# Performance work log

Hardware: AMD Instinct MI355X
Metric: run time of the kernel (lower is better)

The kernel has to match this reference:

```python
import jax, jax.numpy as jnp
import numpy as np

N_NODES = 100000
N_EDGES = 3200000
HID = 64


def setup_inputs() -> dict:
    key = jax.random.key(0)
    ks = jax.random.split(key, 20)
    x = jax.random.normal(ks[0], (N_NODES, 3), dtype=jnp.float32)
    edge_index = jax.random.randint(ks[1], (2, N_EDGES), 0, N_NODES, dtype=jnp.int32)

    def glorot(k, fan_in, fan_out):
        s = jnp.sqrt(6.0 / (fan_in + fan_out))
        return jax.random.uniform(k, (fan_in, fan_out), jnp.float32, -s, s)

    W_in = glorot(ks[2], 3, HID)
    b_in = jnp.zeros((HID,), jnp.float32)
    W_hid = jnp.stack([glorot(ks[3 + i], HID, HID) for i in range(6)])  # [6,64,64]
    b_hid = jnp.zeros((6, HID), jnp.float32)
    W_out = glorot(ks[10], HID, 6)
    b_out = jnp.zeros((6,), jnp.float32)
    return {"x": x, "edge_index": edge_index, "W_in": W_in, "b_in": b_in,
            "W_hid": W_hid, "b_hid": b_hid, "W_out": W_out, "b_out": b_out}


def _gcn_layer(x, W, b, src, dst, norm):
    # PyG GCNConv: h = x @ W; out[dst] += norm * h[src]; out += b
    h = x @ W
    msg = h[src] * norm[:, None]            # [E+N, F]
    agg = jax.ops.segment_sum(msg, dst, num_segments=N_NODES)
    return agg + b


def reference(x, edge_index, W_in, b_in, W_hid, b_hid, W_out, b_out):
    # Add self-loops and symmetric normalization (computed once, shared by all layers)
    loops = jnp.arange(N_NODES, dtype=edge_index.dtype)
    src = jnp.concatenate([edge_index[0], loops])
    dst = jnp.concatenate([edge_index[1], loops])
    deg = jax.ops.segment_sum(jnp.ones_like(dst, dtype=x.dtype), dst, num_segments=N_NODES)
    dinv = jnp.where(deg > 0, jax.lax.rsqrt(deg), 0.0)
    norm = dinv[src] * dinv[dst]            # [E+N]

    h = jax.nn.relu(_gcn_layer(x, W_in, b_in, src, dst, norm))
    for i in range(6):
        h = jax.nn.relu(_gcn_layer(h, W_hid[i], b_hid[i], src, dst, norm))
    # dropout p=0.25 with train=False -> identity (eval mode)
    out = _gcn_layer(h, W_out, b_out, src, dst, norm)
    return jax.nn.sigmoid(out)
```

## Files before the change

kernel.cpp:

```cpp
#include <hip/hip_runtime.h>
#include <hip/hip_fp16.h>
#include <math.h>

#define MAXBKT 512


__global__ __launch_bounds__(256) void k_bcount(const int* __restrict__ dstA,
                                                int E, int N, int nbkt, int* bucketCnt) {
    __shared__ int cnt[MAXBKT];
    for (int i = threadIdx.x; i < nbkt; i += 256) cnt[i] = 0;
    __syncthreads();
    int total = E + N;
    for (int i = blockIdx.x * 256 + threadIdx.x; i < total; i += gridDim.x * 256) {
        int d = (i < E) ? dstA[i] : (i - E);
        atomicAdd(&cnt[d >> 8], 1);
    }
    __syncthreads();
    for (int i = threadIdx.x; i < nbkt; i += 256)
        if (cnt[i]) atomicAdd(&bucketCnt[i], cnt[i]);
}

__global__ __launch_bounds__(MAXBKT) void k_bscan(const int* __restrict__ bucketCnt,
                                                  int* bucketOff, int* bucketCur,
                                                  int nbkt, int total) {
    __shared__ int sm[MAXBKT];
    int tid = threadIdx.x;
    int v = (tid < nbkt) ? bucketCnt[tid] : 0;
    sm[tid] = v;
    __syncthreads();
    for (int off = 1; off < MAXBKT; off <<= 1) {
        int t = 0;
        if (tid >= off) t = sm[tid - off];
        __syncthreads();
        sm[tid] += t;
        __syncthreads();
    }
    if (tid < nbkt) {
        int excl = sm[tid] - v;
        bucketOff[tid] = excl;
        bucketCur[tid] = excl;
    }
    if (tid == 0) bucketOff[nbkt] = total;
}

__global__ __launch_bounds__(256) void k_bscat2(const int* __restrict__ srcA,
                                                const int* __restrict__ dstA,
                                                int* bucketCur, unsigned int* bedges,
                                                int E, int N, int nbkt, int chunk) {
    __shared__ int cnt[MAXBKT];
    __shared__ int base[MAXBKT];
    int total = E + N;
    int lo = blockIdx.x * chunk;
    int hi = lo + chunk; if (hi > total) hi = total;
    for (int i = threadIdx.x; i < nbkt; i += 256) cnt[i] = 0;
    __syncthreads();
    for (int i = lo + threadIdx.x; i < hi; i += 256) {
        int d = (i < E) ? dstA[i] : (i - E);
        atomicAdd(&cnt[d >> 8], 1);
    }
    __syncthreads();
    for (int i = threadIdx.x; i < nbkt; i += 256) {
        base[i] = cnt[i] ? atomicAdd(&bucketCur[i], cnt[i]) : 0;
        cnt[i] = 0;
    }
    __syncthreads();
    for (int i = lo + threadIdx.x; i < hi; i += 256) {
        int s, d;
        if (i < E) { s = srcA[i]; d = dstA[i]; }
        else       { s = d = i - E; }
        int b = d >> 8;
        int pos = base[b] + atomicAdd(&cnt[b], 1);
        bedges[pos] = ((unsigned int)(d & 255) << 24) | (unsigned int)s;
    }
}

__global__ __launch_bounds__(256) void k_bfill2(const unsigned int* __restrict__ bedges,
                                                const int* __restrict__ bucketOff,
                                                const float* __restrict__ x,
                                                int* __restrict__ rowptr,
                                                float* __restrict__ dinv,
                                                float* __restrict__ xs,
                                                int* __restrict__ col,
                                                int N, int total) {
    __shared__ int ldeg[256];
    __shared__ int lcur[256];
    int b = blockIdx.x;
    int tid = threadIdx.x;
    int bo = bucketOff[b], be = bucketOff[b + 1];
    ldeg[tid] = 0;
    __syncthreads();
    for (int j = bo + tid; j < be; j += 256)
        atomicAdd(&ldeg[bedges[j] >> 24], 1);
    __syncthreads();
    int dg = ldeg[tid];
    lcur[tid] = dg;
    __syncthreads();
    for (int off = 1; off < 256; off <<= 1) {
        int t = 0;
        if (tid >= off) t = lcur[tid - off];
        __syncthreads();
        lcur[tid] += t;
        __syncthreads();
    }
    int excl = lcur[tid] - dg;
    int node = (b << 8) + tid;
    if (node < N) {
        rowptr[node] = bo + excl;
        float dv = dg > 0 ? rsqrtf((float)dg) : 0.0f;
        dinv[node] = dv;
        xs[node * 3 + 0] = dv * x[node * 3 + 0];
        xs[node * 3 + 1] = dv * x[node * 3 + 1];
        xs[node * 3 + 2] = dv * x[node * 3 + 2];
    }
    if (b == 0 && tid == 0) rowptr[N] = total;
    __syncthreads();
    lcur[tid] = bo + excl;
    __syncthreads();
    for (int j = bo + tid; j < be; j += 256) {
        unsigned int e = bedges[j];
        int pos = atomicAdd(&lcur[e >> 24], 1);
        col[pos] = (int)(e & 0x00FFFFFFu);
    }
}


__global__ __launch_bounds__(256) void k_agg3(const float* __restrict__ xs,
                                              const int* __restrict__ rowptr,
                                              const int* __restrict__ col,
                                              const float* __restrict__ dinv,
                                              float* __restrict__ out3, int n) {
    int i = blockIdx.x * 256 + threadIdx.x;
    if (i >= n) return;
    float a0 = 0.f, a1 = 0.f, a2 = 0.f;
    int beg = rowptr[i], end = rowptr[i + 1];
    for (int j = beg; j < end; ++j) {
        int s = col[j];
        a0 += xs[s * 3 + 0];
        a1 += xs[s * 3 + 1];
        a2 += xs[s * 3 + 2];
    }
    float dv = dinv[i];
    out3[i * 3 + 0] = dv * a0;
    out3[i * 3 + 1] = dv * a1;
    out3[i * 3 + 2] = dv * a2;
}

__global__ __launch_bounds__(512) void k_tin_mm(const float* __restrict__ agg3v,
                                                const float* __restrict__ Win,
                                                const float* __restrict__ bin,
                                                const float* __restrict__ W0,
                                                const float* __restrict__ dinv,
                                                __half* __restrict__ tout, int n) {
    __shared__ float Wl[64 * 64];
    __shared__ float Hl[8][68];
    int tid = threadIdx.x;
    {
        int i = tid * 4;
        *(float4*)&Wl[i] = *(const float4*)&W0[i];
        *(float4*)&Wl[i + 2048] = *(const float4*)&W0[i + 2048];
    }
    int nodeBase = blockIdx.x * 8;
    int nl = tid >> 6, f = tid & 63;
    int node = nodeBase + nl;
    if (node < n) {
        float a0 = agg3v[node * 3 + 0];
        float a1 = agg3v[node * 3 + 1];
        float a2 = agg3v[node * 3 + 2];
        float v = bin[f] + a0 * Win[f] + a1 * Win[64 + f] + a2 * Win[128 + f];
        Hl[nl][f] = fmaxf(v, 0.f);
    }
    __syncthreads();
    if (node < n) {
        float acc = 0.f;
#pragma unroll
        for (int k = 0; k < 64; ++k) acc += Hl[nl][k] * Wl[k * 64 + f];
        tout[(size_t)node * 64 + f] = __float2half(acc * dinv[node]);
    }
}

__global__ __launch_bounds__(512) void k_aggmm64(const __half* __restrict__ tin,
                                                 const int* __restrict__ rowptr,
                                                 const int* __restrict__ col,
                                                 const float* __restrict__ dinv,
                                                 const float* __restrict__ bias,
                                                 const float* __restrict__ W,
                                                 __half* __restrict__ tnext, int n) {
    __shared__ float Wl[64 * 64];
    __shared__ float Hl[8][68];
    int tid = threadIdx.x;
    {
        int i = tid * 4;
        *(float4*)&Wl[i] = *(const float4*)&W[i];
        *(float4*)&Wl[i + 2048] = *(const float4*)&W[i + 2048];
    }
    int nodeBase = blockIdx.x * 8;
    int wv = tid >> 6;
    int lane = tid & 63;
    int slot = lane >> 3;
    int fl = lane & 7;
    int node = nodeBase + wv;
    float a0 = 0.f, a1 = 0.f, a2 = 0.f, a3 = 0.f, a4 = 0.f, a5 = 0.f, a6 = 0.f, a7 = 0.f;
    if (node < n) {
        int beg = rowptr[node], end = rowptr[node + 1];
        int j = beg + slot;
        for (; j + 24 < end; j += 32) {
            int s0 = col[j], s1 = col[j + 8], s2 = col[j + 16], s3 = col[j + 24];
            float4 r0 = *(const float4*)(tin + (size_t)s0 * 64 + fl * 8);
            float4 r1 = *(const float4*)(tin + (size_t)s1 * 64 + fl * 8);
            float4 r2 = *(const float4*)(tin + (size_t)s2 * 64 + fl * 8);
            float4 r3 = *(const float4*)(tin + (size_t)s3 * 64 + fl * 8);
            const __half2* h0 = (const __half2*)&r0;
            const __half2* h1 = (const __half2*)&r1;
            const __half2* h2 = (const __half2*)&r2;
            const __half2* h3 = (const __half2*)&r3;
            float2 p;
            p = __half22float2(h0[0]); a0 += p.x; a1 += p.y;
            p = __half22float2(h0[1]); a2 += p.x; a3 += p.y;
            p = __half22float2(h0[2]); a4 += p.x; a5 += p.y;
            p = __half22float2(h0[3]); a6 += p.x; a7 += p.y;
            p = __half22float2(h1[0]); a0 += p.x; a1 += p.y;
            p = __half22float2(h1[1]); a2 += p.x; a3 += p.y;
            p = __half22float2(h1[2]); a4 += p.x; a5 += p.y;
            p = __half22float2(h1[3]); a6 += p.x; a7 += p.y;
            p = __half22float2(h2[0]); a0 += p.x; a1 += p.y;
            p = __half22float2(h2[1]); a2 += p.x; a3 += p.y;
            p = __half22float2(h2[2]); a4 += p.x; a5 += p.y;
            p = __half22float2(h2[3]); a6 += p.x; a7 += p.y;
            p = __half22float2(h3[0]); a0 += p.x; a1 += p.y;
            p = __half22float2(h3[1]); a2 += p.x; a3 += p.y;
            p = __half22float2(h3[2]); a4 += p.x; a5 += p.y;
            p = __half22float2(h3[3]); a6 += p.x; a7 += p.y;
        }
        for (; j < end; j += 8) {
            int s0 = col[j];
            float4 r0 = *(const float4*)(tin + (size_t)s0 * 64 + fl * 8);
            const __half2* h0 = (const __half2*)&r0;
            float2 p;
            p = __half22float2(h0[0]); a0 += p.x; a1 += p.y;
            p = __half22float2(h0[1]); a2 += p.x; a3 += p.y;
            p = __half22float2(h0[2]); a4 += p.x; a5 += p.y;
            p = __half22float2(h0[3]); a6 += p.x; a7 += p.y;
        }
    }
#pragma unroll
    for (int m = 8; m < 64; m <<= 1) {
        a0 += __shfl_xor(a0, m, 64);
        a1 += __shfl_xor(a1, m, 64);
        a2 += __shfl_xor(a2, m, 64);
        a3 += __shfl_xor(a3, m, 64);
        a4 += __shfl_xor(a4, m, 64);
        a5 += __shfl_xor(a5, m, 64);
        a6 += __shfl_xor(a6, m, 64);
        a7 += __shfl_xor(a7, m, 64);
    }
    if (slot == 0 && node < n) {
        float dv = dinv[node];
        int fo = fl * 8;
        float4 w0, w1;
        w0.x = fmaxf(dv * a0 + bias[fo + 0], 0.f);
        w0.y = fmaxf(dv * a1 + bias[fo + 1], 0.f);
        w0.z = fmaxf(dv * a2 + bias[fo + 2], 0.f);
        w0.w = fmaxf(dv * a3 + bias[fo + 3], 0.f);
        w1.x = fmaxf(dv * a4 + bias[fo + 4], 0.f);
        w1.y = fmaxf(dv * a5 + bias[fo + 5], 0.f);
        w1.z = fmaxf(dv * a6 + bias[fo + 6], 0.f);
        w1.w = fmaxf(dv * a7 + bias[fo + 7], 0.f);
        *(float4*)&Hl[wv][fo] = w0;
        *(float4*)&Hl[wv][fo + 4] = w1;
    }
    __syncthreads();
    if (node < n) {
        int f = lane;
        float acc = 0.f;
#pragma unroll
        for (int k = 0; k < 64; ++k) acc += Hl[wv][k] * Wl[k * 64 + f];
        tnext[(size_t)node * 64 + f] = __float2half(acc * dinv[node]);
    }
}

__global__ __launch_bounds__(512) void k_aggtout(const __half* __restrict__ tin,
                                                 const int* __restrict__ rowptr,
                                                 const int* __restrict__ col,
                                                 const float* __restrict__ dinv,
                                                 const float* __restrict__ bias,
                                                 const float* __restrict__ Wout,
                                                 __half* __restrict__ t6p, int n) {
    __shared__ float Wl6[64 * 6];
    __shared__ float Hl[8][68];
    int tid = threadIdx.x;
    if (tid < 384) Wl6[tid] = Wout[tid];
    int nodeBase = blockIdx.x * 8;
    int wv = tid >> 6;
    int lane = tid & 63;
    int slot = lane >> 3;
    int fl = lane & 7;
    int node = nodeBase + wv;
    float a0 = 0.f, a1 = 0.f, a2 = 0.f, a3 = 0.f, a4 = 0.f, a5 = 0.f, a6 = 0.f, a7 = 0.f;
    if (node < n) {
        int beg = rowptr[node], end = rowptr[node + 1];
        int j = beg + slot;
        for (; j + 24 < end; j += 32) {
            int s0 = col[j], s1 = col[j + 8], s2 = col[j + 16], s3 = col[j + 24];
            float4 r0 = *(const float4*)(tin + (size_t)s0 * 64 + fl * 8);
            float4 r1 = *(const float4*)(tin + (size_t)s1 * 64 + fl * 8);
            float4 r2 = *(const float4*)(tin + (size_t)s2 * 64 + fl * 8);
            float4 r3 = *(const float4*)(tin + (size_t)s3 * 64 + fl * 8);
            const __half2* h0 = (const __half2*)&r0;
            const __half2* h1 = (const __half2*)&r1;
            const __half2* h2 = (const __half2*)&r2;
            const __half2* h3 = (const __half2*)&r3;
            float2 p;
            p = __half22float2(h0[0]); a0 += p.x; a1 += p.y;
            p = __half22float2(h0[1]); a2 += p.x; a3 += p.y;
            p = __half22float2(h0[2]); a4 += p.x; a5 += p.y;
            p = __half22float2(h0[3]); a6 += p.x; a7 += p.y;
            p = __half22float2(h1[0]); a0 += p.x; a1 += p.y;
            p = __half22float2(h1[1]); a2 += p.x; a3 += p.y;
            p = __half22float2(h1[2]); a4 += p.x; a5 += p.y;
            p = __half22float2(h1[3]); a6 += p.x; a7 += p.y;
            p = __half22float2(h2[0]); a0 += p.x; a1 += p.y;
            p = __half22float2(h2[1]); a2 += p.x; a3 += p.y;
            p = __half22float2(h2[2]); a4 += p.x; a5 += p.y;
            p = __half22float2(h2[3]); a6 += p.x; a7 += p.y;
            p = __half22float2(h3[0]); a0 += p.x; a1 += p.y;
            p = __half22float2(h3[1]); a2 += p.x; a3 += p.y;
            p = __half22float2(h3[2]); a4 += p.x; a5 += p.y;
            p = __half22float2(h3[3]); a6 += p.x; a7 += p.y;
        }
        for (; j < end; j += 8) {
            int s0 = col[j];
            float4 r0 = *(const float4*)(tin + (size_t)s0 * 64 + fl * 8);
            const __half2* h0 = (const __half2*)&r0;
            float2 p;
            p = __half22float2(h0[0]); a0 += p.x; a1 += p.y;
            p = __half22float2(h0[1]); a2 += p.x; a3 += p.y;
            p = __half22float2(h0[2]); a4 += p.x; a5 += p.y;
            p = __half22float2(h0[3]); a6 += p.x; a7 += p.y;
        }
    }
#pragma unroll
    for (int m = 8; m < 64; m <<= 1) {
        a0 += __shfl_xor(a0, m, 64);
        a1 += __shfl_xor(a1, m, 64);
        a2 += __shfl_xor(a2, m, 64);
        a3 += __shfl_xor(a3, m, 64);
        a4 += __shfl_xor(a4, m, 64);
        a5 += __shfl_xor(a5, m, 64);
        a6 += __shfl_xor(a6, m, 64);
        a7 += __shfl_xor(a7, m, 64);
    }
    if (slot == 0 && node < n) {
        float dv = dinv[node];
        int fo = fl * 8;
        float4 w0, w1;
        w0.x = fmaxf(dv * a0 + bias[fo + 0], 0.f);
        w0.y = fmaxf(dv * a1 + bias[fo + 1], 0.f);
        w0.z = fmaxf(dv * a2 + bias[fo + 2], 0.f);
        w0.w = fmaxf(dv * a3 + bias[fo + 3], 0.f);
        w1.x = fmaxf(dv * a4 + bias[fo + 4], 0.f);
        w1.y = fmaxf(dv * a5 + bias[fo + 5], 0.f);
        w1.z = fmaxf(dv * a6 + bias[fo + 6], 0.f);
        w1.w = fmaxf(dv * a7 + bias[fo + 7], 0.f);
        *(float4*)&Hl[wv][fo] = w0;
        *(float4*)&Hl[wv][fo + 4] = w1;
    }
    __syncthreads();
    if (node < n && lane < 8) {
        __half o = __float2half(0.f);
        if (lane < 6) {
            float acc = 0.f;
#pragma unroll
            for (int k = 0; k < 64; ++k) acc += Hl[wv][k] * Wl6[k * 6 + lane];
            o = __float2half(acc * dinv[node]);
        }
        t6p[(size_t)node * 8 + lane] = o;
    }
}

__global__ __launch_bounds__(256) void k_agg6(const __half* __restrict__ t6p,
                                              const int* __restrict__ rowptr,
                                              const int* __restrict__ col,
                                              const float* __restrict__ dinv,
                                              const float* __restrict__ bout,
                                              float* __restrict__ out, int n) {
    int i = blockIdx.x * 256 + threadIdx.x;
    if (i >= n) return;
    float a0 = 0.f, a1 = 0.f, a2 = 0.f, a3 = 0.f, a4 = 0.f, a5 = 0.f;
    int beg = rowptr[i], end = rowptr[i + 1];
    int j = beg;
    for (; j + 1 < end; j += 2) {
        int s0 = col[j], s1 = col[j + 1];
        float4 r0 = *(const float4*)(t6p + (size_t)s0 * 8);
        float4 r1 = *(const float4*)(t6p + (size_t)s1 * 8);
        const __half2* h0 = (const __half2*)&r0;
        const __half2* h1 = (const __half2*)&r1;
        float2 p;
        p = __half22float2(h0[0]); a0 += p.x; a1 += p.y;
        p = __half22float2(h0[1]); a2 += p.x; a3 += p.y;
        p = __half22float2(h0[2]); a4 += p.x; a5 += p.y;
        p = __half22float2(h1[0]); a0 += p.x; a1 += p.y;
        p = __half22float2(h1[1]); a2 += p.x; a3 += p.y;
        p = __half22float2(h1[2]); a4 += p.x; a5 += p.y;
    }
    if (j < end) {
        int s0 = col[j];
        float4 r0 = *(const float4*)(t6p + (size_t)s0 * 8);
        const __half2* h0 = (const __half2*)&r0;
        float2 p;
        p = __half22float2(h0[0]); a0 += p.x; a1 += p.y;
        p = __half22float2(h0[1]); a2 += p.x; a3 += p.y;
        p = __half22float2(h0[2]); a4 += p.x; a5 += p.y;
    }
    float dv = dinv[i];
    out[i * 6 + 0] = 1.0f / (1.0f + expf(-(dv * a0 + bout[0])));
    out[i * 6 + 1] = 1.0f / (1.0f + expf(-(dv * a1 + bout[1])));
    out[i * 6 + 2] = 1.0f / (1.0f + expf(-(dv * a2 + bout[2])));
    out[i * 6 + 3] = 1.0f / (1.0f + expf(-(dv * a3 + bout[3])));
    out[i * 6 + 4] = 1.0f / (1.0f + expf(-(dv * a4 + bout[4])));
    out[i * 6 + 5] = 1.0f / (1.0f + expf(-(dv * a5 + bout[5])));
}


extern "C" void kernel_launch(void* const* d_in, const int* in_sizes, int n_in,
                              void* d_out, int out_size, void* d_ws, size_t ws_size,
                              hipStream_t stream) {
    const float* x    = (const float*)d_in[0];
    const int*   eidx = (const int*)d_in[1];
    const float* Win  = (const float*)d_in[2];
    const float* bin  = (const float*)d_in[3];
    const float* Whid = (const float*)d_in[4];
    const float* bhid = (const float*)d_in[5];
    const float* Wout = (const float*)d_in[6];
    const float* bout = (const float*)d_in[7];
    float* out = (float*)d_out;

    const int N = in_sizes[0] / 3;
    const int E = in_sizes[1] / 2;
    const int* srcA = eidx;
    const int* dstA = eidx + E;
    const int TOT = E + N;
    const int NBKT = (N + 255) >> 8;

    char* p = (char*)d_ws;
    auto alloc = [&](size_t bytes) -> void* {
        void* r = (void*)p;
        p += (bytes + 255) & ~(size_t)255;
        return r;
    };
    float*        dinv      = (float*)alloc((size_t)N * 4);
    int*          rowptr    = (int*)alloc((size_t)(N + 1) * 4);
    int*          bucketCnt = (int*)alloc((size_t)MAXBKT * 4);
    int*          bucketOff = (int*)alloc((size_t)(MAXBKT + 1) * 4);
    int*          bucketCur = (int*)alloc((size_t)MAXBKT * 4);
    unsigned int* bedges    = (unsigned int*)alloc((size_t)TOT * 4);
    int*          col       = (int*)alloc((size_t)TOT * 4);
    float*        xs        = (float*)alloc((size_t)N * 3 * 4);
    float*        agg3buf   = (float*)alloc((size_t)N * 3 * 4);
    __half*       tA        = (__half*)alloc((size_t)N * 64 * 2);
    __half*       tB        = (__half*)alloc((size_t)N * 64 * 2);
    __half*       t6p       = (__half*)alloc((size_t)N * 8 * 2);

    const int NB_N = (N + 255) / 256;
    const int NB8  = (N + 7) / 8;

    hipMemsetAsync(bucketCnt, 0, (size_t)MAXBKT * 4, stream);
    k_bcount<<<512, 256, 0, stream>>>(dstA, E, N, NBKT, bucketCnt);
    k_bscan<<<1, MAXBKT, 0, stream>>>(bucketCnt, bucketOff, bucketCur, NBKT, TOT);
    const int CHUNK = (TOT + 511) / 512;
    k_bscat2<<<512, 256, 0, stream>>>(srcA, dstA, bucketCur, bedges, E, N, NBKT, CHUNK);
    k_bfill2<<<NBKT, 256, 0, stream>>>(bedges, bucketOff, x, rowptr, dinv, xs, col, N, TOT);

    k_agg3<<<NB_N, 256, 0, stream>>>(xs, rowptr, col, dinv, agg3buf, N);
    k_tin_mm<<<NB8, 512, 0, stream>>>(agg3buf, Win, bin, Whid, dinv, tA, N);

    __half* tin = tA;
    __half* tnx = tB;
    for (int i = 1; i <= 5; ++i) {
        k_aggmm64<<<NB8, 512, 0, stream>>>(tin, rowptr, col, dinv,
                                           bhid + (size_t)(i - 1) * 64,
                                           Whid + (size_t)i * 4096, tnx, N);
        __half* tmp = tin; tin = tnx; tnx = tmp;
    }

    k_aggtout<<<NB8, 512, 0, stream>>>(tin, rowptr, col, dinv,
                                       bhid + (size_t)5 * 64, Wout, t6p, N);

    k_agg6<<<NB_N, 256, 0, stream>>>(t6p, rowptr, col, dinv, bout, out, N);
}
```

Measured before the change: 770.5 us.

## Keep layer weights in registers and drop shared-memory matmul in fused agg kernels

The fused aggregate+matmul kernels stop staging the 64x64 weight matrix and the aggregated row in LDS. Each lane now holds an 8x8 slice of W (as half2) plus its bias in registers, and computes the per-node transform with a shuffle reduction. This removes the 16KB LDS fill per block and the block-wide barrier, and blocks shrink to 4 nodes of 256 threads. In exchange it adds register pressure, rounds the weights to fp16, and every block re-reads W from global/cache.

```diff
diff --git a/kernel.cpp b/kernel.cpp
--- a/kernel.cpp
+++ b/kernel.cpp
@@ -178,69 +178,72 @@
     }
 }
 
-__global__ __launch_bounds__(512) void k_aggmm64(const __half* __restrict__ tin,
+__global__ __launch_bounds__(256) void k_aggmm64(const __half* __restrict__ tin,
                                                  const int* __restrict__ rowptr,
                                                  const int* __restrict__ col,
                                                  const float* __restrict__ dinv,
                                                  const float* __restrict__ bias,
                                                  const float* __restrict__ W,
                                                  __half* __restrict__ tnext, int n) {
-    __shared__ float Wl[64 * 64];
-    __shared__ float Hl[8][68];
     int tid = threadIdx.x;
-    {
-        int i = tid * 4;
-        *(float4*)&Wl[i] = *(const float4*)&W[i];
-        *(float4*)&Wl[i + 2048] = *(const float4*)&W[i + 2048];
-    }
-    int nodeBase = blockIdx.x * 8;
-    int wv = tid >> 6;
     int lane = tid & 63;
     int slot = lane >> 3;
-    int fl = lane & 7;
-    int node = nodeBase + wv;
+    int fl   = lane & 7;
+    __half2 w2[8][4];
+    float biasreg[8];
+#pragma unroll
+    for (int q = 0; q < 8; ++q) {
+        const float* wrow = W + (fl * 8 + q) * 64 + slot * 8;
+        float4 wa = *(const float4*)wrow;
+        float4 wb = *(const float4*)(wrow + 4);
+        w2[q][0] = __floats2half2_rn(wa.x, wa.y);
+        w2[q][1] = __floats2half2_rn(wa.z, wa.w);
+        w2[q][2] = __floats2half2_rn(wb.x, wb.y);
+        w2[q][3] = __floats2half2_rn(wb.z, wb.w);
+        biasreg[q] = bias[fl * 8 + q];
+    }
+    int node = blockIdx.x * 4 + (tid >> 6);
+    if (node >= n) return;
+    int beg = rowptr[node], end = rowptr[node + 1];
     float a0 = 0.f, a1 = 0.f, a2 = 0.f, a3 = 0.f, a4 = 0.f, a5 = 0.f, a6 = 0.f, a7 = 0.f;
-    if (node < n) {
-        int beg = rowptr[node], end = rowptr[node + 1];
-        int j = beg + slot;
-        for (; j + 24 < end; j += 32) {
-            int s0 = col[j], s1 = col[j + 8], s2 = col[j + 16], s3 = col[j + 24];
-            float4 r0 = *(const float4*)(tin + (size_t)s0 * 64 + fl * 8);
-            float4 r1 = *(const float4*)(tin + (size_t)s1 * 64 + fl * 8);
-            float4 r2 = *(const float4*)(tin + (size_t)s2 * 64 + fl * 8);
-            float4 r3 = *(const float4*)(tin + (size_t)s3 * 64 + fl * 8);
-            const __half2* h0 = (const __half2*)&r0;
-            const __half2* h1 = (const __half2*)&r1;
-            const __half2* h2 = (const __half2*)&r2;
-            const __half2* h3 = (const __half2*)&r3;
-            float2 p;
-            p = __half22float2(h0[0]); a0 += p.x; a1 += p.y;
-            p = __half22float2(h0[1]); a2 += p.x; a3 += p.y;
-            p = __half22float2(h0[2]); a4 += p.x; a5 += p.y;
-            p = __half22float2(h0[3]); a6 += p.x; a7 += p.y;
-            p = __half22float2(h1[0]); a0 += p.x; a1 += p.y;
-            p = __half22float2(h1[1]); a2 += p.x; a3 += p.y;
-            p = __half22float2(h1[2]); a4 += p.x; a5 += p.y;
-            p = __half22float2(h1[3]); a6 += p.x; a7 += p.y;
-            p = __half22float2(h2[0]); a0 += p.x; a1 += p.y;
-            p = __half22float2(h2[1]); a2 += p.x; a3 += p.y;
-            p = __half22float2(h2[2]); a4 += p.x; a5 += p.y;
-            p = __half22float2(h2[3]); a6 += p.x; a7 += p.y;
-            p = __half22float2(h3[0]); a0 += p.x; a1 += p.y;
-            p = __half22float2(h3[1]); a2 += p.x; a3 += p.y;
-            p = __half22float2(h3[2]); a4 += p.x; a5 += p.y;
-            p = __half22float2(h3[3]); a6 += p.x; a7 += p.y;
-        }
-        for (; j < end; j += 8) {
-            int s0 = col[j];
-            float4 r0 = *(const float4*)(tin + (size_t)s0 * 64 + fl * 8);
-            const __half2* h0 = (const __half2*)&r0;
-            float2 p;
-            p = __half22float2(h0[0]); a0 += p.x; a1 += p.y;
-            p = __half22float2(h0[1]); a2 += p.x; a3 += p.y;
-            p = __half22float2(h0[2]); a4 += p.x; a5 += p.y;
-            p = __half22float2(h0[3]); a6 += p.x; a7 += p.y;
-        }
+    int j = beg + slot;
+    for (; j + 24 < end; j += 32) {
+        int s0 = col[j], s1 = col[j + 8], s2 = col[j + 16], s3 = col[j + 24];
+        float4 r0 = *(const float4*)(tin + (size_t)s0 * 64 + fl * 8);
+        float4 r1 = *(const float4*)(tin + (size_t)s1 * 64 + fl * 8);
+        float4 r2 = *(const float4*)(tin + (size_t)s2 * 64 + fl * 8);
+        float4 r3 = *(const float4*)(tin + (size_t)s3 * 64 + fl * 8);
+        const __half2* h0 = (const __half2*)&r0;
+        const __half2* h1 = (const __half2*)&r1;
+        const __half2* h2 = (const __half2*)&r2;
+        const __half2* h3 = (const __half2*)&r3;
+        float2 p;
+        p = __half22float2(h0[0]); a0 += p.x; a1 += p.y;
+        p = __half22float2(h0[1]); a2 += p.x; a3 += p.y;
+        p = __half22float2(h0[2]); a4 += p.x; a5 += p.y;
+        p = __half22float2(h0[3]); a6 += p.x; a7 += p.y;
+        p = __half22float2(h1[0]); a0 += p.x; a1 += p.y;
+        p = __half22float2(h1[1]); a2 += p.x; a3 += p.y;
+        p = __half22float2(h1[2]); a4 += p.x; a5 += p.y;
+        p = __half22float2(h1[3]); a6 += p.x; a7 += p.y;
+        p = __half22float2(h2[0]); a0 += p.x; a1 += p.y;
+        p = __half22float2(h2[1]); a2 += p.x; a3 += p.y;
+        p = __half22float2(h2[2]); a4 += p.x; a5 += p.y;
+        p = __half22float2(h2[3]); a6 += p.x; a7 += p.y;
+        p = __half22float2(h3[0]); a0 += p.x; a1 += p.y;
+        p = __half22float2(h3[1]); a2 += p.x; a3 += p.y;
+        p = __half22float2(h3[2]); a4 += p.x; a5 += p.y;
+        p = __half22float2(h3[3]); a6 += p.x; a7 += p.y;
+    }
+    for (; j < end; j += 8) {
+        int s0 = col[j];
+        float4 r0 = *(const float4*)(tin + (size_t)s0 * 64 + fl * 8);
+        const __half2* h0 = (const __half2*)&r0;
+        float2 p;
+        p = __half22float2(h0[0]); a0 += p.x; a1 += p.y;
+        p = __half22float2(h0[1]); a2 += p.x; a3 += p.y;
+        p = __half22float2(h0[2]); a4 += p.x; a5 += p.y;
+        p = __half22float2(h0[3]); a6 += p.x; a7 += p.y;
     }
 #pragma unroll
     for (int m = 8; m < 64; m <<= 1) {
@@ -253,90 +256,102 @@
         a6 += __shfl_xor(a6, m, 64);
         a7 += __shfl_xor(a7, m, 64);
     }
-    if (slot == 0 && node < n) {
-        float dv = dinv[node];
-        int fo = fl * 8;
-        float4 w0, w1;
-        w0.x = fmaxf(dv * a0 + bias[fo + 0], 0.f);
-        w0.y = fmaxf(dv * a1 + bias[fo + 1], 0.f);
-        w0.z = fmaxf(dv * a2 + bias[fo + 2], 0.f);
-        w0.w = fmaxf(dv * a3 + bias[fo + 3], 0.f);
-        w1.x = fmaxf(dv * a4 + bias[fo + 4], 0.f);
-        w1.y = fmaxf(dv * a5 + bias[fo + 5], 0.f);
-        w1.z = fmaxf(dv * a6 + bias[fo + 6], 0.f);
-        w1.w = fmaxf(dv * a7 + bias[fo + 7], 0.f);
-        *(float4*)&Hl[wv][fo] = w0;
-        *(float4*)&Hl[wv][fo + 4] = w1;
-    }
-    __syncthreads();
-    if (node < n) {
-        int f = lane;
-        float acc = 0.f;
-#pragma unroll
-        for (int k = 0; k < 64; ++k) acc += Hl[wv][k] * Wl[k * 64 + f];
-        tnext[(size_t)node * 64 + f] = __float2half(acc * dinv[node]);
-    }
-}
-
-__global__ __launch_bounds__(512) void k_aggtout(const __half* __restrict__ tin,
+    float dv = dinv[node];
+    float h[8];
+    h[0] = fmaxf(dv * a0 + biasreg[0], 0.f);
+    h[1] = fmaxf(dv * a1 + biasreg[1], 0.f);
+    h[2] = fmaxf(dv * a2 + biasreg[2], 0.f);
+    h[3] = fmaxf(dv * a3 + biasreg[3], 0.f);
+    h[4] = fmaxf(dv * a4 + biasreg[4], 0.f);
+    h[5] = fmaxf(dv * a5 + biasreg[5], 0.f);
+    h[6] = fmaxf(dv * a6 + biasreg[6], 0.f);
+    h[7] = fmaxf(dv * a7 + biasreg[7], 0.f);
+    float acc[8] = {0.f, 0.f, 0.f, 0.f, 0.f, 0.f, 0.f, 0.f};
+#pragma unroll
+    for (int q = 0; q < 8; ++q) {
+        float hq = h[q];
+#pragma unroll
+        for (int p2 = 0; p2 < 4; ++p2) {
+            float2 wf = __half22float2(w2[q][p2]);
+            acc[2 * p2]     += hq * wf.x;
+            acc[2 * p2 + 1] += hq * wf.y;
+        }
+    }
+#pragma unroll
+    for (int m = 1; m < 8; m <<= 1) {
+#pragma unroll
+        for (int p = 0; p < 8; ++p) acc[p] += __shfl_xor(acc[p], m, 64);
+    }
+    if (fl == 0) {
+        __half2 o[4];
+        o[0] = __floats2half2_rn(acc[0] * dv, acc[1] * dv);
+        o[1] = __floats2half2_rn(acc[2] * dv, acc[3] * dv);
+        o[2] = __floats2half2_rn(acc[4] * dv, acc[5] * dv);
+        o[3] = __floats2half2_rn(acc[6] * dv, acc[7] * dv);
+        *(float4*)&tnext[(size_t)node * 64 + slot * 8] = *(float4*)o;
+    }
+}
+
+__global__ __launch_bounds__(256) void k_aggtout(const __half* __restrict__ tin,
                                                  const int* __restrict__ rowptr,
                                                  const int* __restrict__ col,
                                                  const float* __restrict__ dinv,
                                                  const float* __restrict__ bias,
                                                  const float* __restrict__ Wout,
                                                  __half* __restrict__ t6p, int n) {
-    __shared__ float Wl6[64 * 6];
-    __shared__ float Hl[8][68];
     int tid = threadIdx.x;
-    if (tid < 384) Wl6[tid] = Wout[tid];
-    int nodeBase = blockIdx.x * 8;
-    int wv = tid >> 6;
     int lane = tid & 63;
     int slot = lane >> 3;
-    int fl = lane & 7;
-    int node = nodeBase + wv;
+    int fl   = lane & 7;
+    float woutreg[8];
+    float biasreg[8];
+#pragma unroll
+    for (int q = 0; q < 8; ++q) {
+        woutreg[q] = (slot < 6) ? Wout[(fl * 8 + q) * 6 + slot] : 0.f;
+        biasreg[q] = bias[fl * 8 + q];
+    }
+    int node = blockIdx.x * 4 + (tid >> 6);
+    if (node >= n) return;
+    int beg = rowptr[node], end = rowptr[node + 1];
     float a0 = 0.f, a1 = 0.f, a2 = 0.f, a3 = 0.f, a4 = 0.f, a5 = 0.f, a6 = 0.f, a7 = 0.f;
-    if (node < n) {
-        int beg = rowptr[node], end = rowptr[node + 1];
-        int j = beg + slot;
-        for (; j + 24 < end; j += 32) {
-            int s0 = col[j], s1 = col[j + 8], s2 = col[j + 16], s3 = col[j + 24];
-            float4 r0 = *(const float4*)(tin + (size_t)s0 * 64 + fl * 8);
-            float4 r1 = *(const float4*)(tin + (size_t)s1 * 64 + fl * 8);
-            float4 r2 = *(const float4*)(tin + (size_t)s2 * 64 + fl * 8);
-            float4 r3 = *(const float4*)(tin + (size_t)s3 * 64 + fl * 8);
-            const __half2* h0 = (const __half2*)&r0;
-            const __half2* h1 = (const __half2*)&r1;
-            const __half2* h2 = (const __half2*)&r2;
-            const __half2* h3 = (const __half2*)&r3;
-            float2 p;
-            p = __half22float2(h0[0]); a0 += p.x; a1 += p.y;
-            p = __half22float2(h0[1]); a2 += p.x; a3 += p.y;
-            p = __half22float2(h0[2]); a4 += p.x; a5 += p.y;
-            p = __half22float2(h0[3]); a6 += p.x; a7 += p.y;
-            p = __half22float2(h1[0]); a0 += p.x; a1 += p.y;
-            p = __half22float2(h1[1]); a2 += p.x; a3 += p.y;
-            p = __half22float2(h1[2]); a4 += p.x; a5 += p.y;
-            p = __half22float2(h1[3]); a6 += p.x; a7 += p.y;
-            p = __half22float2(h2[0]); a0 += p.x; a1 += p.y;
-            p = __half22float2(h2[1]); a2 += p.x; a3 += p.y;
-            p = __half22float2(h2[2]); a4 += p.x; a5 += p.y;
-            p = __half22float2(h2[3]); a6 += p.x; a7 += p.y;
-            p = __half22float2(h3[0]); a0 += p.x; a1 += p.y;
-            p = __half22float2(h3[1]); a2 += p.x; a3 += p.y;
-            p = __half22float2(h3[2]); a4 += p.x; a5 += p.y;
-            p = __half22float2(h3[3]); a6 += p.x; a7 += p.y;
-        }
-        for (; j < end; j += 8) {
-            int s0 = col[j];
-            float4 r0 = *(const float4*)(tin + (size_t)s0 * 64 + fl * 8);
-            const __half2* h0 = (const __half2*)&r0;
-            float2 p;
-            p = __half22float2(h0[0]); a0 += p.x; a1 += p.y;
-            p = __half22float2(h0[1]); a2 += p.x; a3 += p.y;
-            p = __half22float2(h0[2]); a4 += p.x; a5 += p.y;
-            p = __half22float2(h0[3]); a6 += p.x; a7 += p.y;
-        }
+    int j = beg + slot;
+    for (; j + 24 < end; j += 32) {
+        int s0 = col[j], s1 = col[j + 8], s2 = col[j + 16], s3 = col[j + 24];
+        float4 r0 = *(const float4*)(tin + (size_t)s0 * 64 + fl * 8);
+        float4 r1 = *(const float4*)(tin + (size_t)s1 * 64 + fl * 8);
+        float4 r2 = *(const float4*)(tin + (size_t)s2 * 64 + fl * 8);
+        float4 r3 = *(const float4*)(tin + (size_t)s3 * 64 + fl * 8);
+        const __half2* h0 = (const __half2*)&r0;
+        const __half2* h1 = (const __half2*)&r1;
+        const __half2* h2 = (const __half2*)&r2;
+        const __half2* h3 = (const __half2*)&r3;
+        float2 p;
+        p = __half22float2(h0[0]); a0 += p.x; a1 += p.y;
+        p = __half22float2(h0[1]); a2 += p.x; a3 += p.y;
+        p = __half22float2(h0[2]); a4 += p.x; a5 += p.y;
+        p = __half22float2(h0[3]); a6 += p.x; a7 += p.y;
+        p = __half22float2(h1[0]); a0 += p.x; a1 += p.y;
+        p = __half22float2(h1[1]); a2 += p.x; a3 += p.y;
+        p = __half22float2(h1[2]); a4 += p.x; a5 += p.y;
+        p = __half22float2(h1[3]); a6 += p.x; a7 += p.y;
+        p = __half22float2(h2[0]); a0 += p.x; a1 += p.y;
+        p = __half22float2(h2[1]); a2 += p.x; a3 += p.y;
+        p = __half22float2(h2[2]); a4 += p.x; a5 += p.y;
+        p = __half22float2(h2[3]); a6 += p.x; a7 += p.y;
+        p = __half22float2(h3[0]); a0 += p.x; a1 += p.y;
+        p = __half22float2(h3[1]); a2 += p.x; a3 += p.y;
+        p = __half22float2(h3[2]); a4 += p.x; a5 += p.y;
+        p = __half22float2(h3[3]); a6 += p.x; a7 += p.y;
+    }
+    for (; j < end; j += 8) {
+        int s0 = col[j];
+        float4 r0 = *(const float4*)(tin + (size_t)s0 * 64 + fl * 8);
+        const __half2* h0 = (const __half2*)&r0;
+        float2 p;
+        p = __half22float2(h0[0]); a0 += p.x; a1 += p.y;
+        p = __half22float2(h0[1]); a2 += p.x; a3 += p.y;
+        p = __half22float2(h0[2]); a4 += p.x; a5 += p.y;
+        p = __half22float2(h0[3]); a6 += p.x; a7 += p.y;
     }
 #pragma unroll
     for (int m = 8; m < 64; m <<= 1) {
@@ -349,32 +364,23 @@
         a6 += __shfl_xor(a6, m, 64);
         a7 += __shfl_xor(a7, m, 64);
     }
-    if (slot == 0 && node < n) {
-        float dv = dinv[node];
-        int fo = fl * 8;
-        float4 w0, w1;
-        w0.x = fmaxf(dv * a0 + bias[fo + 0], 0.f);
-        w0.y = fmaxf(dv * a1 + bias[fo + 1], 0.f);
-        w0.z = fmaxf(dv * a2 + bias[fo + 2], 0.f);
-        w0.w = fmaxf(dv * a3 + bias[fo + 3], 0.f);
-        w1.x = fmaxf(dv * a4 + bias[fo + 4], 0.f);
-        w1.y = fmaxf(dv * a5 + bias[fo + 5], 0.f);
-        w1.z = fmaxf(dv * a6 + bias[fo + 6], 0.f);
-        w1.w = fmaxf(dv * a7 + bias[fo + 7], 0.f);
-        *(float4*)&Hl[wv][fo] = w0;
-        *(float4*)&Hl[wv][fo + 4] = w1;
-    }
-    __syncthreads();
-    if (node < n && lane < 8) {
-        __half o = __float2half(0.f);
-        if (lane < 6) {
-            float acc = 0.f;
-#pragma unroll
-            for (int k = 0; k < 64; ++k) acc += Hl[wv][k] * Wl6[k * 6 + lane];
-            o = __float2half(acc * dinv[node]);
-        }
-        t6p[(size_t)node * 8 + lane] = o;
-    }
+    float dv = dinv[node];
+    float h[8];
+    h[0] = fmaxf(dv * a0 + biasreg[0], 0.f);
+    h[1] = fmaxf(dv * a1 + biasreg[1], 0.f);
+    h[2] = fmaxf(dv * a2 + biasreg[2], 0.f);
+    h[3] = fmaxf(dv * a3 + biasreg[3], 0.f);
+    h[4] = fmaxf(dv * a4 + biasreg[4], 0.f);
+    h[5] = fmaxf(dv * a5 + biasreg[5], 0.f);
+    h[6] = fmaxf(dv * a6 + biasreg[6], 0.f);
+    h[7] = fmaxf(dv * a7 + biasreg[7], 0.f);
+    float part = 0.f;
+#pragma unroll
+    for (int q = 0; q < 8; ++q) part += h[q] * woutreg[q];
+#pragma unroll
+    for (int m = 1; m < 8; m <<= 1) part += __shfl_xor(part, m, 64);
+    if (fl == 0)
+        t6p[(size_t)node * 8 + slot] = __float2half((slot < 6) ? part * dv : 0.f);
 }
 
 __global__ __launch_bounds__(256) void k_agg6(const __half* __restrict__ t6p,
@@ -461,6 +467,7 @@
     __half*       t6p       = (__half*)alloc((size_t)N * 8 * 2);
 
     const int NB_N = (N + 255) / 256;
+    const int NB4  = (N + 3) / 4;
     const int NB8  = (N + 7) / 8;
 
     hipMemsetAsync(bucketCnt, 0, (size_t)MAXBKT * 4, stream);
@@ -476,13 +483,13 @@
     __half* tin = tA;
     __half* tnx = tB;
     for (int i = 1; i <= 5; ++i) {
-        k_aggmm64<<<NB8, 512, 0, stream>>>(tin, rowptr, col, dinv,
+        k_aggmm64<<<NB4, 256, 0, stream>>>(tin, rowptr, col, dinv,
                                            bhid + (size_t)(i - 1) * 64,
                                            Whid + (size_t)i * 4096, tnx, N);
         __half* tmp = tin; tin = tnx; tnx = tmp;
     }
 
-    k_aggtout<<<NB8, 512, 0, stream>>>(tin, rowptr, col, dinv,
+    k_aggtout<<<NB4, 256, 0, stream>>>(tin, rowptr, col, dinv,
                                        bhid + (size_t)5 * 64, Wout, t6p, N);
 
     k_agg6<<<NB_N, 256, 0, stream>>>(t6p, rowptr, col, dinv, bout, out, N);
```

New measurement: 1.605 ms. +108.3%, slower.
